# Performance work log

Measured on AMD Instinct MI355X. Metric: run time of the kernel, lower is better.

## Reference

```python
import jax, jax.numpy as jnp
import numpy as np

N_NODES = 100000


def gcn_layer(x, W, b, src, dst, n):
    # add self loops
    loop = jnp.arange(n, dtype=src.dtype)
    s = jnp.concatenate([src, loop])
    d = jnp.concatenate([dst, loop])
    # degree computed over row (source) of edge_index with self loops,
    # matching PyG degree(row, size[0])
    deg = jax.ops.segment_sum(jnp.ones_like(s, dtype=x.dtype), s, num_segments=n)
    dinv = jax.lax.rsqrt(deg)  # self loops guarantee deg >= 1
    h = x @ W + b  # [n, out]
    norm = dinv[s] * dinv[d]  # [E+n]
    msg = norm[:, None] * h[s]  # gather from source nodes
    return jax.ops.segment_sum(msg, d, num_segments=n)  # scatter-add to targets


def setup_inputs() -> dict:
    key = jax.random.key(0)
    k1, k2, k3, k4 = jax.random.split(key, 4)
    nfeat, nhid, nclass = 512, 16, 40
    E = 3200000
    x = jax.random.normal(k1, (N_NODES, nfeat), dtype=jnp.float32)
    edge_index = jax.random.randint(k2, (2, E), 0, N_NODES, dtype=jnp.int64)
    W1 = jax.random.normal(k3, (nfeat, nhid), dtype=jnp.float32) * (1.0 / np.sqrt(nfeat))
    b1 = jnp.zeros((nhid,), dtype=jnp.float32)
    W2 = jax.random.normal(k4, (nhid, nclass), dtype=jnp.float32) * (1.0 / np.sqrt(nhid))
    b2 = jnp.zeros((nclass,), dtype=jnp.float32)
    return {"x": x, "edge_index": edge_index, "W1": W1, "b1": b1, "W2": W2, "b2": b2}


def reference(x, edge_index, W1, b1, W2, b2):
    n = x.shape[0]
    src, dst = edge_index[0], edge_index[1]
    h = gcn_layer(x, W1, b1, src, dst, n)
    h = jax.nn.relu(h)
    # dropout: eval mode (identity), matching F.dropout(training=False)
    h = gcn_layer(h, W2, b2, src, dst, n)
    return jax.nn.log_softmax(h, axis=1)
```

## Files before the change

kernel.cpp:

```cpp
#include <hip/hip_runtime.h>
#include <hip/hip_bf16.h>

#define BSH 9
#define BSZ 512
#define CAP 17408
#define CHK 4096

typedef __attribute__((ext_vector_type(8))) short bf16x8;
typedef __attribute__((ext_vector_type(4))) float f32x4;

__device__ __forceinline__ unsigned short f2bf(float f) {
    unsigned u = __float_as_uint(f);
    u += 0x7fffu + ((u >> 16) & 1u);
    return (unsigned short)(u >> 16);
}
__device__ __forceinline__ float b2f(unsigned short v) {
    return __uint_as_float((unsigned)v << 16);
}

__global__ void init_k(int* __restrict__ curD, int* __restrict__ curS, int nbk) {
    int i = threadIdx.x;
    if (i < nbk) { curD[i] = i * CAP; curS[i] = i * CAP; }
}


#define GROWS 64
#define GKC 256
#define GSTR 264

__global__ __launch_bounds__(256) void fused_gs_k(
    const float* __restrict__ X, const float* __restrict__ W, const float* __restrict__ B,
    float* __restrict__ H, int n, int nGm,
    const int* __restrict__ src, const int* __restrict__ dst, int E,
    int* __restrict__ curD, int* __restrict__ curS,
    unsigned int* __restrict__ pairs, unsigned short* __restrict__ sbuf, int nbk) {
    __shared__ char smem[GROWS * GSTR * 2];
    int t = threadIdx.x;

    if ((int)blockIdx.x < nGm) {
        unsigned short* xt = (unsigned short*)smem;
        int lane = t & 63, wave = t >> 6;
        int rowBase = blockIdx.x * GROWS;
        int bn = lane & 15;

        {
            int kt0 = t >> 4, kg0 = (t >> 2) & 3, bn0 = (t & 3) * 4;
            unsigned short frag[4][8];
#pragma unroll
            for (int j = 0; j < 8; ++j) {
                float4 w = *(const float4*)&W[(size_t)(kt0 * 32 + kg0 * 8 + j) * 16 + bn0];
                frag[0][j] = f2bf(w.x); frag[1][j] = f2bf(w.y);
                frag[2][j] = f2bf(w.z); frag[3][j] = f2bf(w.w);
            }
#pragma unroll
            for (int b = 0; b < 4; ++b)
                *(uint4*)&xt[((kt0 * 4 + kg0) * 16 + bn0 + b) * 8] = *(const uint4*)frag[b];
        }
        __syncthreads();
        bf16x8 bw[16];
#pragma unroll
        for (int kt = 0; kt < 16; ++kt)
            bw[kt] = *(const bf16x8*)&xt[(kt * 64 + lane) * 8];
        float bias = B[bn];
        __syncthreads();

        f32x4 acc = {0.f, 0.f, 0.f, 0.f};
        int srow = t >> 4, skq = t & 15;

        for (int ch = 0; ch < 2; ++ch) {
#pragma unroll
            for (int p = 0; p < 4; ++p) {
                int r = p * 16 + srow;
                int gr = rowBase + r;
                const float* xr = &X[(size_t)(gr < n ? gr : n - 1) * 512 + ch * GKC + skq * 4];
#pragma unroll
                for (int q = 0; q < 4; ++q) {
                    float4 v = *(const float4*)&xr[q * 64];
                    ushort4 u;
                    u.x = f2bf(v.x); u.y = f2bf(v.y); u.z = f2bf(v.z); u.w = f2bf(v.w);
                    *(ushort4*)&xt[r * GSTR + skq * 4 + q * 64] = u;
                }
            }
            __syncthreads();

            int rb = (wave * 16 + bn) * GSTR + (lane >> 4) * 8;
#pragma unroll
            for (int kt = 0; kt < 8; ++kt) {
                bf16x8 af = *(const bf16x8*)&xt[rb + kt * 32];
                acc = __builtin_amdgcn_mfma_f32_16x16x32_bf16(af, bw[ch * 8 + kt], acc, 0, 0, 0);
            }
            __syncthreads();
        }

        int r0 = rowBase + wave * 16 + (lane >> 4) * 4;
#pragma unroll
        for (int i = 0; i < 4; ++i) {
            int row = r0 + i;
            if (row < n) H[(size_t)row * 16 + bn] = acc[i] + bias;
        }
    } else {
        unsigned int*   stageD = (unsigned int*)smem;
        unsigned short* stageS = (unsigned short*)(smem + 16384);
        int* cntD  = (int*)(smem + 24576);
        int* cntS  = (int*)(smem + 25600);
        int* rsvD  = (int*)(smem + 26624);
        int* rsvS  = (int*)(smem + 27648);
        int* scanD = (int*)(smem + 28672);
        int* scanS = (int*)(smem + 29696);
        int* ps    = (int*)(smem + 30720);

        int bb = blockIdx.x - nGm;
        int lo = bb * CHK, hi = min(E, lo + CHK);
        bool full = (hi - lo) == CHK;

        cntD[t] = 0; cntS[t] = 0;
        __syncthreads();

        int sv[16], dv[16];
        if (full) {
#pragma unroll
            for (int j = 0; j < 16; j++) {
                int i = lo + t + j * 256;
                sv[j] = src[i]; dv[j] = dst[i];
            }
#pragma unroll
            for (int j = 0; j < 16; j++) {
                atomicAdd(&cntD[dv[j] >> BSH], 1);
                atomicAdd(&cntS[sv[j] >> BSH], 1);
            }
        } else {
            for (int i = lo + t; i < hi; i += 256) {
                atomicAdd(&cntD[dst[i] >> BSH], 1);
                atomicAdd(&cntS[src[i] >> BSH], 1);
            }
        }
        __syncthreads();
        int vD = cntD[t];
        ps[t] = vD; __syncthreads();
        for (int o = 1; o < 256; o <<= 1) {
            int u = (t >= o) ? ps[t - o] : 0; __syncthreads();
            ps[t] += u; __syncthreads();
        }
        scanD[t] = ps[t] - vD;
        if (t < nbk && vD) rsvD[t] = atomicAdd(&curD[t], vD);
        __syncthreads();
        int vS = cntS[t];
        ps[t] = vS; __syncthreads();
        for (int o = 1; o < 256; o <<= 1) {
            int u = (t >= o) ? ps[t - o] : 0; __syncthreads();
            ps[t] += u; __syncthreads();
        }
        scanS[t] = ps[t] - vS;
        if (t < nbk && vS) rsvS[t] = atomicAdd(&curS[t], vS);
        cntD[t] = 0; cntS[t] = 0;
        __syncthreads();
        if (full) {
#pragma unroll
            for (int j = 0; j < 16; j++) {
                int s = sv[j], d = dv[j];
                int bd = d >> BSH;
                int pd = scanD[bd] + atomicAdd(&cntD[bd], 1);
                stageD[pd] = ((unsigned int)s << BSH) | (unsigned int)(d & (BSZ - 1));
                int bs = s >> BSH;
                int pp = scanS[bs] + atomicAdd(&cntS[bs], 1);
                stageS[pp] = (unsigned short)(s & (BSZ - 1));
            }
        } else {
            for (int i = lo + t; i < hi; i += 256) {
                int s = src[i], d = dst[i];
                int bd = d >> BSH;
                int pd = scanD[bd] + atomicAdd(&cntD[bd], 1);
                stageD[pd] = ((unsigned int)s << BSH) | (unsigned int)(d & (BSZ - 1));
                int bs = s >> BSH;
                int pp = scanS[bs] + atomicAdd(&cntS[bs], 1);
                stageS[pp] = (unsigned short)(s & (BSZ - 1));
            }
        }
        __syncthreads();
        int wave = t >> 6, lane = t & 63;
        for (int b = wave; b < nbk; b += 4) {
            int st = scanD[b], len = cntD[b], g = rsvD[b];
            for (int j = lane; j < len; j += 64) pairs[g + j] = stageD[st + j];
        }
        for (int b = wave; b < nbk; b += 4) {
            int st = scanS[b], len = cntS[b], g = rsvS[b];
            for (int j = lane; j < len; j += 64) sbuf[g + j] = stageS[st + j];
        }
    }
}


__global__ __launch_bounds__(256) void dinvScale_k(const unsigned short* __restrict__ sbuf,
                                                   const int* __restrict__ curS,
                                                   const float* __restrict__ h1,
                                                   float* __restrict__ dinv,
                                                   unsigned short* __restrict__ hw1, int n) {
    __shared__ int cnt[BSZ];
    __shared__ float dl[BSZ];
    int b = blockIdx.x, t = threadIdx.x;
    cnt[t] = 0; cnt[t + 256] = 0;
    __syncthreads();
    int lo = b * CAP, hi = curS[b];
    for (int i = lo + t; i < hi; i += 256) atomicAdd(&cnt[sbuf[i]], 1);
    __syncthreads();
    int n0 = b * BSZ + t, n1 = n0 + 256;
    float d0 = rsqrtf((float)(1 + cnt[t]));
    float d1 = rsqrtf((float)(1 + cnt[t + 256]));
    dl[t] = d0; dl[t + 256] = d1;
    if (n0 < n) dinv[n0] = d0;
    if (n1 < n) dinv[n1] = d1;
    __syncthreads();
    int rows = min(BSZ, n - b * BSZ);
    int lim4 = rows * 4;
    size_t base = (size_t)b * BSZ * 16;
#pragma unroll
    for (int j = 0; j < 8; j++) {
        int i4 = j * 256 + t;
        if (i4 < lim4) {
            float4 v = *(const float4*)&h1[base + (size_t)i4 * 4];
            float d = dl[i4 >> 2];
            ushort4 u;
            u.x = f2bf(v.x * d); u.y = f2bf(v.y * d);
            u.z = f2bf(v.z * d); u.w = f2bf(v.w * d);
            *(ushort4*)&hw1[base + (size_t)i4 * 4] = u;
        }
    }
}


#define FPS 65536.f
#define FPI (1.f / 65536.f)

template <int LAYER>
__global__ __launch_bounds__(1024) void aggB_k(
    const unsigned int* __restrict__ pairs, const int* __restrict__ curD,
    const unsigned short* __restrict__ HW, const float* __restrict__ dinv,
    float* __restrict__ rowsum, const float* __restrict__ W2,
    const float* __restrict__ B2, unsigned short* __restrict__ outA,
    float* __restrict__ outF, int n, int nc) {
    __shared__ int iacc[BSZ * 16];
    __shared__ unsigned int rsl[BSZ];
    int b = blockIdx.x, t = threadIdx.x;
    for (int i = t; i < BSZ * 16; i += 1024) iacc[i] = 0;
    if (LAYER == 1 && t < BSZ) rsl[t] = 0u;
    __syncthreads();

    int lo = b * CAP, hi = curD[b];
    int q = t & 3;
    int i = lo + (t >> 2);
    for (; i + 768 < hi; i += 1024) {
        unsigned int p0 = pairs[i], p1 = pairs[i + 256];
        unsigned int p2 = pairs[i + 512], p3 = pairs[i + 768];
        int s0 = p0 >> BSH, l0 = p0 & (BSZ - 1);
        int s1 = p1 >> BSH, l1 = p1 & (BSZ - 1);
        int s2 = p2 >> BSH, l2 = p2 & (BSZ - 1);
        int s3 = p3 >> BSH, l3 = p3 & (BSZ - 1);
        ushort4 u0 = *(const ushort4*)&HW[(size_t)s0 * 16 + q * 4];
        ushort4 u1 = *(const ushort4*)&HW[(size_t)s1 * 16 + q * 4];
        ushort4 u2 = *(const ushort4*)&HW[(size_t)s2 * 16 + q * 4];
        ushort4 u3 = *(const ushort4*)&HW[(size_t)s3 * 16 + q * 4];
        int* a0 = &iacc[l0 * 16 + q * 4];
        atomicAdd(&a0[0], __float2int_rn(b2f(u0.x) * FPS));
        atomicAdd(&a0[1], __float2int_rn(b2f(u0.y) * FPS));
        atomicAdd(&a0[2], __float2int_rn(b2f(u0.z) * FPS));
        atomicAdd(&a0[3], __float2int_rn(b2f(u0.w) * FPS));
        int* a1 = &iacc[l1 * 16 + q * 4];
        atomicAdd(&a1[0], __float2int_rn(b2f(u1.x) * FPS));
        atomicAdd(&a1[1], __float2int_rn(b2f(u1.y) * FPS));
        atomicAdd(&a1[2], __float2int_rn(b2f(u1.z) * FPS));
        atomicAdd(&a1[3], __float2int_rn(b2f(u1.w) * FPS));
        int* a2 = &iacc[l2 * 16 + q * 4];
        atomicAdd(&a2[0], __float2int_rn(b2f(u2.x) * FPS));
        atomicAdd(&a2[1], __float2int_rn(b2f(u2.y) * FPS));
        atomicAdd(&a2[2], __float2int_rn(b2f(u2.z) * FPS));
        atomicAdd(&a2[3], __float2int_rn(b2f(u2.w) * FPS));
        int* a3 = &iacc[l3 * 16 + q * 4];
        atomicAdd(&a3[0], __float2int_rn(b2f(u3.x) * FPS));
        atomicAdd(&a3[1], __float2int_rn(b2f(u3.y) * FPS));
        atomicAdd(&a3[2], __float2int_rn(b2f(u3.z) * FPS));
        atomicAdd(&a3[3], __float2int_rn(b2f(u3.w) * FPS));
        if (LAYER == 1 && q == 0) {
            atomicAdd(&rsl[l0], (unsigned int)(dinv[s0] * FPS + 0.5f));
            atomicAdd(&rsl[l1], (unsigned int)(dinv[s1] * FPS + 0.5f));
            atomicAdd(&rsl[l2], (unsigned int)(dinv[s2] * FPS + 0.5f));
            atomicAdd(&rsl[l3], (unsigned int)(dinv[s3] * FPS + 0.5f));
        }
    }
    for (; i < hi; i += 256) {
        unsigned int p0 = pairs[i];
        int s0 = p0 >> BSH, l0 = p0 & (BSZ - 1);
        ushort4 u0 = *(const ushort4*)&HW[(size_t)s0 * 16 + q * 4];
        int* a0 = &iacc[l0 * 16 + q * 4];
        atomicAdd(&a0[0], __float2int_rn(b2f(u0.x) * FPS));
        atomicAdd(&a0[1], __float2int_rn(b2f(u0.y) * FPS));
        atomicAdd(&a0[2], __float2int_rn(b2f(u0.z) * FPS));
        atomicAdd(&a0[3], __float2int_rn(b2f(u0.w) * FPS));
        if (LAYER == 1 && q == 0) atomicAdd(&rsl[l0], (unsigned int)(dinv[s0] * FPS + 0.5f));
    }
    __syncthreads();

    if (LAYER == 1) {
        int ln = t >> 1, f0 = (t & 1) * 8;
        int node = b * BSZ + ln;
        if (node < n) {
            float dd = dinv[node];
            const ushort4* sp = (const ushort4*)&HW[(size_t)node * 16 + f0];
            ushort4 s0 = sp[0], s1 = sp[1];
            const int* ap = &iacc[ln * 16 + f0];
            ushort4 o0, o1;
            o0.x = f2bf(dd * fmaxf(dd * ((float)ap[0] * FPI + b2f(s0.x)), 0.f));
            o0.y = f2bf(dd * fmaxf(dd * ((float)ap[1] * FPI + b2f(s0.y)), 0.f));
            o0.z = f2bf(dd * fmaxf(dd * ((float)ap[2] * FPI + b2f(s0.z)), 0.f));
            o0.w = f2bf(dd * fmaxf(dd * ((float)ap[3] * FPI + b2f(s0.w)), 0.f));
            o1.x = f2bf(dd * fmaxf(dd * ((float)ap[4] * FPI + b2f(s1.x)), 0.f));
            o1.y = f2bf(dd * fmaxf(dd * ((float)ap[5] * FPI + b2f(s1.y)), 0.f));
            o1.z = f2bf(dd * fmaxf(dd * ((float)ap[6] * FPI + b2f(s1.z)), 0.f));
            o1.w = f2bf(dd * fmaxf(dd * ((float)ap[7] * FPI + b2f(s1.w)), 0.f));
            ushort4* op = (ushort4*)&outA[(size_t)node * 16 + f0];
            op[0] = o0; op[1] = o1;
            if (f0 == 0) rowsum[node] = dd * (dd + (float)rsl[ln] * FPI);
        }
    } else {
        int wave = t >> 6, lane = t & 63;
        int node0 = b * BSZ;
        int nodeEnd = min(node0 + BSZ, n);
        for (int node = node0 + wave; node < nodeEnd; node += 16) {
            int ln = node - node0;
            float dd = dinv[node];
            float f[16];
            const ushort4* sp = (const ushort4*)&HW[(size_t)node * 16];
#pragma unroll
            for (int g = 0; g < 4; g++) {
                ushort4 u = sp[g];
                f[g * 4 + 0] = dd * ((float)iacc[ln * 16 + g * 4 + 0] * FPI + b2f(u.x));
                f[g * 4 + 1] = dd * ((float)iacc[ln * 16 + g * 4 + 1] * FPI + b2f(u.y));
                f[g * 4 + 2] = dd * ((float)iacc[ln * 16 + g * 4 + 2] * FPI + b2f(u.z));
                f[g * 4 + 3] = dd * ((float)iacc[ln * 16 + g * 4 + 3] * FPI + b2f(u.w));
            }
            float logit = -1e30f;
            if (lane < nc) {
                logit = rowsum[node] * B2[lane];
#pragma unroll
                for (int k = 0; k < 16; k++) logit = fmaf(f[k], W2[k * nc + lane], logit);
            }
            float m = logit;
#pragma unroll
            for (int off = 1; off < 64; off <<= 1) m = fmaxf(m, __shfl_xor(m, off, 64));
            float e = (lane < nc) ? __expf(logit - m) : 0.f;
            float s = e;
#pragma unroll
            for (int off = 1; off < 64; off <<= 1) s += __shfl_xor(s, off, 64);
            if (lane < nc) outF[(size_t)node * nc + lane] = logit - m - __logf(s);
        }
    }
}


extern "C" void kernel_launch(void* const* d_in, const int* in_sizes, int n_in,
                              void* d_out, int out_size, void* d_ws, size_t ws_size,
                              hipStream_t stream) {
    const float* X  = (const float*)d_in[0];
    const int*   EI = (const int*)d_in[1];
    const float* W1 = (const float*)d_in[2];
    const float* B1 = (const float*)d_in[3];
    const float* W2 = (const float*)d_in[4];
    const float* B2 = (const float*)d_in[5];
    float* out = (float*)d_out;

    int NH = in_sizes[3];
    int NC = in_sizes[5];
    int NF = in_sizes[2] / NH;
    int n  = in_sizes[0] / NF;
    int E  = in_sizes[1] / 2;
    const int* src = EI;
    const int* dst = EI + E;
    int nbk = (n + BSZ - 1) >> BSH;

    char* ws = (char*)d_ws;
    size_t o = 0;
    auto alloc = [&](size_t bytes) { size_t r = o; o = (o + bytes + 255) & ~(size_t)255; return r; };
    size_t o_dinv   = alloc((size_t)n * 4);
    size_t o_rsum   = alloc((size_t)n * 4);
    size_t o_curD   = alloc(1024);
    size_t o_curS   = alloc(1024);
    size_t o_pairs  = alloc((size_t)nbk * CAP * 4);
    size_t o_sbuf   = alloc((size_t)nbk * CAP * 2);
    size_t o_h1     = alloc((size_t)n * 16 * 4);
    size_t o_hw1    = alloc((size_t)n * 16 * 2);
    size_t o_a1w    = alloc((size_t)n * 16 * 2);

    float* dinv  = (float*)(ws + o_dinv);
    float* rsum  = (float*)(ws + o_rsum);
    int* curD    = (int*)(ws + o_curD);
    int* curS    = (int*)(ws + o_curS);
    unsigned int* pairs   = (unsigned int*)(ws + o_pairs);
    unsigned short* sbuf  = (unsigned short*)(ws + o_sbuf);
    float* h1    = (float*)(ws + o_h1);
    unsigned short* hw1 = (unsigned short*)(ws + o_hw1);
    unsigned short* a1w = (unsigned short*)(ws + o_a1w);

    init_k<<<1, 256, 0, stream>>>(curD, curS, nbk);

    int NBLK = (E + CHK - 1) / CHK;
    int nGm = (n + GROWS - 1) / GROWS;
    fused_gs_k<<<nGm + NBLK, 256, 0, stream>>>(X, W1, B1, h1, n, nGm,
                                               src, dst, E, curD, curS,
                                               pairs, sbuf, nbk);
    dinvScale_k<<<nbk, 256, 0, stream>>>(sbuf, curS, h1, dinv, hw1, n);

    aggB_k<1><<<nbk, 1024, 0, stream>>>(pairs, curD, hw1, dinv, rsum,
                                        nullptr, nullptr, a1w, nullptr, n, NC);
    aggB_k<2><<<nbk, 1024, 0, stream>>>(pairs, curD, a1w, dinv, rsum,
                                        W2, B2, nullptr, out, n, NC);
}
```

Before: 197.9 us.

## Split fused GEMM/scatter kernel and use shuffle-based block scan

```diff
diff --git a/kernel.cpp b/kernel.cpp
--- a/kernel.cpp
+++ b/kernel.cpp
@@ -23,169 +23,177 @@
     if (i < nbk) { curD[i] = i * CAP; curS[i] = i * CAP; }
 }
 
+__device__ __forceinline__ int blockExclScan(int v, int t, int* wsum) {
+    int lane = t & 63, wv = t >> 6;
+    int x = v;
+#pragma unroll
+    for (int off = 1; off < 64; off <<= 1) {
+        int y = __shfl_up(x, off, 64);
+        if (lane >= off) x += y;
+    }
+    if (lane == 63) wsum[wv] = x;
+    __syncthreads();
+    int prefix = 0;
+#pragma unroll
+    for (int w = 0; w < 4; ++w) prefix += (w < wv) ? wsum[w] : 0;
+    return x + prefix - v;
+}
+
+
+__global__ __launch_bounds__(256) void scatter_k(
+    const int* __restrict__ src, const int* __restrict__ dst, int E,
+    int* __restrict__ curD, int* __restrict__ curS,
+    unsigned int* __restrict__ pairs, unsigned short* __restrict__ sbuf, int nbk) {
+    __shared__ char smem[32512];
+    unsigned int*   stageD = (unsigned int*)smem;
+    unsigned short* stageS = (unsigned short*)(smem + 16384);
+    int* cntD  = (int*)(smem + 24576);
+    int* cntS  = (int*)(smem + 25600);
+    int* rsvD  = (int*)(smem + 26624);
+    int* rsvS  = (int*)(smem + 27648);
+    int* scanD = (int*)(smem + 28672);
+    int* scanS = (int*)(smem + 29696);
+    int* wsum  = (int*)(smem + 30720);
+    int t = threadIdx.x;
+
+    int lo = blockIdx.x * CHK, hi = min(E, lo + CHK);
+    bool full = (hi - lo) == CHK;
+
+    cntD[t] = 0; cntS[t] = 0;
+    __syncthreads();
+
+    int sv[16], dv[16];
+    if (full) {
+#pragma unroll
+        for (int j = 0; j < 16; j++) {
+            int i = lo + t + j * 256;
+            sv[j] = src[i]; dv[j] = dst[i];
+        }
+#pragma unroll
+        for (int j = 0; j < 16; j++) {
+            atomicAdd(&cntD[dv[j] >> BSH], 1);
+            atomicAdd(&cntS[sv[j] >> BSH], 1);
+        }
+    } else {
+        for (int i = lo + t; i < hi; i += 256) {
+            atomicAdd(&cntD[dst[i] >> BSH], 1);
+            atomicAdd(&cntS[src[i] >> BSH], 1);
+        }
+    }
+    __syncthreads();
+    int vD = cntD[t];
+    int vS = cntS[t];
+    int eD = blockExclScan(vD, t, wsum);
+    __syncthreads();
+    int eS = blockExclScan(vS, t, wsum);
+    scanD[t] = eD;
+    scanS[t] = eS;
+    if (t < nbk && vD) rsvD[t] = atomicAdd(&curD[t], vD);
+    if (t < nbk && vS) rsvS[t] = atomicAdd(&curS[t], vS);
+    cntD[t] = 0; cntS[t] = 0;
+    __syncthreads();
+    if (full) {
+#pragma unroll
+        for (int j = 0; j < 16; j++) {
+            int s = sv[j], d = dv[j];
+            int bd = d >> BSH;
+            int pd = scanD[bd] + atomicAdd(&cntD[bd], 1);
+            stageD[pd] = ((unsigned int)s << BSH) | (unsigned int)(d & (BSZ - 1));
+            int bs = s >> BSH;
+            int pp = scanS[bs] + atomicAdd(&cntS[bs], 1);
+            stageS[pp] = (unsigned short)(s & (BSZ - 1));
+        }
+    } else {
+        for (int i = lo + t; i < hi; i += 256) {
+            int s = src[i], d = dst[i];
+            int bd = d >> BSH;
+            int pd = scanD[bd] + atomicAdd(&cntD[bd], 1);
+            stageD[pd] = ((unsigned int)s << BSH) | (unsigned int)(d & (BSZ - 1));
+            int bs = s >> BSH;
+            int pp = scanS[bs] + atomicAdd(&cntS[bs], 1);
+            stageS[pp] = (unsigned short)(s & (BSZ - 1));
+        }
+    }
+    __syncthreads();
+    int wave = t >> 6, lane = t & 63;
+    for (int b = wave; b < nbk; b += 4) {
+        int st = scanD[b], len = cntD[b], g = rsvD[b];
+        for (int j = lane; j < len; j += 64) pairs[g + j] = stageD[st + j];
+    }
+    for (int b = wave; b < nbk; b += 4) {
+        int st = scanS[b], len = cntS[b], g = rsvS[b];
+        for (int j = lane; j < len; j += 64) sbuf[g + j] = stageS[st + j];
+    }
+}
+
 
 #define GROWS 64
 #define GKC 256
 #define GSTR 264
 
-__global__ __launch_bounds__(256) void fused_gs_k(
+__global__ __launch_bounds__(256) void gemm_k(
     const float* __restrict__ X, const float* __restrict__ W, const float* __restrict__ B,
-    float* __restrict__ H, int n, int nGm,
-    const int* __restrict__ src, const int* __restrict__ dst, int E,
-    int* __restrict__ curD, int* __restrict__ curS,
-    unsigned int* __restrict__ pairs, unsigned short* __restrict__ sbuf, int nbk) {
-    __shared__ char smem[GROWS * GSTR * 2];
+    float* __restrict__ H, int n) {
+    __shared__ unsigned short xt[GROWS * GSTR];
     int t = threadIdx.x;
-
-    if ((int)blockIdx.x < nGm) {
-        unsigned short* xt = (unsigned short*)smem;
-        int lane = t & 63, wave = t >> 6;
-        int rowBase = blockIdx.x * GROWS;
-        int bn = lane & 15;
-
-        {
-            int kt0 = t >> 4, kg0 = (t >> 2) & 3, bn0 = (t & 3) * 4;
-            unsigned short frag[4][8];
-#pragma unroll
-            for (int j = 0; j < 8; ++j) {
-                float4 w = *(const float4*)&W[(size_t)(kt0 * 32 + kg0 * 8 + j) * 16 + bn0];
-                frag[0][j] = f2bf(w.x); frag[1][j] = f2bf(w.y);
-                frag[2][j] = f2bf(w.z); frag[3][j] = f2bf(w.w);
+    int lane = t & 63, wave = t >> 6;
+    int rowBase = blockIdx.x * GROWS;
+    int bn = lane & 15;
+
+    {
+        int kt0 = t >> 4, kg0 = (t >> 2) & 3, bn0 = (t & 3) * 4;
+        unsigned short frag[4][8];
+#pragma unroll
+        for (int j = 0; j < 8; ++j) {
+            float4 w = *(const float4*)&W[(size_t)(kt0 * 32 + kg0 * 8 + j) * 16 + bn0];
+            frag[0][j] = f2bf(w.x); frag[1][j] = f2bf(w.y);
+            frag[2][j] = f2bf(w.z); frag[3][j] = f2bf(w.w);
+        }
+#pragma unroll
+        for (int b = 0; b < 4; ++b)
+            *(uint4*)&xt[((kt0 * 4 + kg0) * 16 + bn0 + b) * 8] = *(const uint4*)frag[b];
+    }
+    __syncthreads();
+    bf16x8 bw[16];
+#pragma unroll
+    for (int kt = 0; kt < 16; ++kt)
+        bw[kt] = *(const bf16x8*)&xt[(kt * 64 + lane) * 8];
+    float bias = B[bn];
+    __syncthreads();
+
+    f32x4 acc = {0.f, 0.f, 0.f, 0.f};
+    int srow = t >> 4, skq = t & 15;
+
+    for (int ch = 0; ch < 2; ++ch) {
+#pragma unroll
+        for (int p = 0; p < 4; ++p) {
+            int r = p * 16 + srow;
+            int gr = rowBase + r;
+            const float* xr = &X[(size_t)(gr < n ? gr : n - 1) * 512 + ch * GKC + skq * 4];
+#pragma unroll
+            for (int q = 0; q < 4; ++q) {
+                float4 v = *(const float4*)&xr[q * 64];
+                ushort4 u;
+                u.x = f2bf(v.x); u.y = f2bf(v.y); u.z = f2bf(v.z); u.w = f2bf(v.w);
+                *(ushort4*)&xt[r * GSTR + skq * 4 + q * 64] = u;
             }
-#pragma unroll
-            for (int b = 0; b < 4; ++b)
-                *(uint4*)&xt[((kt0 * 4 + kg0) * 16 + bn0 + b) * 8] = *(const uint4*)frag[b];
         }
         __syncthreads();
-        bf16x8 bw[16];
-#pragma unroll
-        for (int kt = 0; kt < 16; ++kt)
-            bw[kt] = *(const bf16x8*)&xt[(kt * 64 + lane) * 8];
-        float bias = B[bn];
+
+        int rb = (wave * 16 + bn) * GSTR + (lane >> 4) * 8;
+#pragma unroll
+        for (int kt = 0; kt < 8; ++kt) {
+            bf16x8 af = *(const bf16x8*)&xt[rb + kt * 32];
+            acc = __builtin_amdgcn_mfma_f32_16x16x32_bf16(af, bw[ch * 8 + kt], acc, 0, 0, 0);
+        }
         __syncthreads();
-
-        f32x4 acc = {0.f, 0.f, 0.f, 0.f};
-        int srow = t >> 4, skq = t & 15;
-
-        for (int ch = 0; ch < 2; ++ch) {
-#pragma unroll
-            for (int p = 0; p < 4; ++p) {
-                int r = p * 16 + srow;
-                int gr = rowBase + r;
-                const float* xr = &X[(size_t)(gr < n ? gr : n - 1) * 512 + ch * GKC + skq * 4];
-#pragma unroll
-                for (int q = 0; q < 4; ++q) {
-                    float4 v = *(const float4*)&xr[q * 64];
-                    ushort4 u;
-                    u.x = f2bf(v.x); u.y = f2bf(v.y); u.z = f2bf(v.z); u.w = f2bf(v.w);
-                    *(ushort4*)&xt[r * GSTR + skq * 4 + q * 64] = u;
-                }
-            }
-            __syncthreads();
-
-            int rb = (wave * 16 + bn) * GSTR + (lane >> 4) * 8;
-#pragma unroll
-            for (int kt = 0; kt < 8; ++kt) {
-                bf16x8 af = *(const bf16x8*)&xt[rb + kt * 32];
-                acc = __builtin_amdgcn_mfma_f32_16x16x32_bf16(af, bw[ch * 8 + kt], acc, 0, 0, 0);
-            }
-            __syncthreads();
-        }
-
-        int r0 = rowBase + wave * 16 + (lane >> 4) * 4;
-#pragma unroll
-        for (int i = 0; i < 4; ++i) {
-            int row = r0 + i;
-            if (row < n) H[(size_t)row * 16 + bn] = acc[i] + bias;
-        }
-    } else {
-        unsigned int*   stageD = (unsigned int*)smem;
-        unsigned short* stageS = (unsigned short*)(smem + 16384);
-        int* cntD  = (int*)(smem + 24576);
-        int* cntS  = (int*)(smem + 25600);
-        int* rsvD  = (int*)(smem + 26624);
-        int* rsvS  = (int*)(smem + 27648);
-        int* scanD = (int*)(smem + 28672);
-        int* scanS = (int*)(smem + 29696);
-        int* ps    = (int*)(smem + 30720);
-
-        int bb = blockIdx.x - nGm;
-        int lo = bb * CHK, hi = min(E, lo + CHK);
-        bool full = (hi - lo) == CHK;
-
-        cntD[t] = 0; cntS[t] = 0;
-        __syncthreads();
-
-        int sv[16], dv[16];
-        if (full) {
-#pragma unroll
-            for (int j = 0; j < 16; j++) {
-                int i = lo + t + j * 256;
-                sv[j] = src[i]; dv[j] = dst[i];
-            }
-#pragma unroll
-            for (int j = 0; j < 16; j++) {
-                atomicAdd(&cntD[dv[j] >> BSH], 1);
-                atomicAdd(&cntS[sv[j] >> BSH], 1);
-            }
-        } else {
-            for (int i = lo + t; i < hi; i += 256) {
-                atomicAdd(&cntD[dst[i] >> BSH], 1);
-                atomicAdd(&cntS[src[i] >> BSH], 1);
-            }
-        }
-        __syncthreads();
-        int vD = cntD[t];
-        ps[t] = vD; __syncthreads();
-        for (int o = 1; o < 256; o <<= 1) {
-            int u = (t >= o) ? ps[t - o] : 0; __syncthreads();
-            ps[t] += u; __syncthreads();
-        }
-        scanD[t] = ps[t] - vD;
-        if (t < nbk && vD) rsvD[t] = atomicAdd(&curD[t], vD);
-        __syncthreads();
-        int vS = cntS[t];
-        ps[t] = vS; __syncthreads();
-        for (int o = 1; o < 256; o <<= 1) {
-            int u = (t >= o) ? ps[t - o] : 0; __syncthreads();
-            ps[t] += u; __syncthreads();
-        }
-        scanS[t] = ps[t] - vS;
-        if (t < nbk && vS) rsvS[t] = atomicAdd(&curS[t], vS);
-        cntD[t] = 0; cntS[t] = 0;
-        __syncthreads();
-        if (full) {
-#pragma unroll
-            for (int j = 0; j < 16; j++) {
-                int s = sv[j], d = dv[j];
-                int bd = d >> BSH;
-                int pd = scanD[bd] + atomicAdd(&cntD[bd], 1);
-                stageD[pd] = ((unsigned int)s << BSH) | (unsigned int)(d & (BSZ - 1));
-                int bs = s >> BSH;
-                int pp = scanS[bs] + atomicAdd(&cntS[bs], 1);
-                stageS[pp] = (unsigned short)(s & (BSZ - 1));
-            }
-        } else {
-            for (int i = lo + t; i < hi; i += 256) {
-                int s = src[i], d = dst[i];
-                int bd = d >> BSH;
-                int pd = scanD[bd] + atomicAdd(&cntD[bd], 1);
-                stageD[pd] = ((unsigned int)s << BSH) | (unsigned int)(d & (BSZ - 1));
-                int bs = s >> BSH;
-                int pp = scanS[bs] + atomicAdd(&cntS[bs], 1);
-                stageS[pp] = (unsigned short)(s & (BSZ - 1));
-            }
-        }
-        __syncthreads();
-        int wave = t >> 6, lane = t & 63;
-        for (int b = wave; b < nbk; b += 4) {
-            int st = scanD[b], len = cntD[b], g = rsvD[b];
-            for (int j = lane; j < len; j += 64) pairs[g + j] = stageD[st + j];
-        }
-        for (int b = wave; b < nbk; b += 4) {
-            int st = scanS[b], len = cntS[b], g = rsvS[b];
-            for (int j = lane; j < len; j += 64) sbuf[g + j] = stageS[st + j];
-        }
+    }
+
+    int r0 = rowBase + wave * 16 + (lane >> 4) * 4;
+#pragma unroll
+    for (int i = 0; i < 4; ++i) {
+        int row = r0 + i;
+        if (row < n) H[(size_t)row * 16 + bn] = acc[i] + bias;
     }
 }
 
@@ -403,9 +411,8 @@
 
     int NBLK = (E + CHK - 1) / CHK;
     int nGm = (n + GROWS - 1) / GROWS;
-    fused_gs_k<<<nGm + NBLK, 256, 0, stream>>>(X, W1, B1, h1, n, nGm,
-                                               src, dst, E, curD, curS,
-                                               pairs, sbuf, nbk);
+    scatter_k<<<NBLK, 256, 0, stream>>>(src, dst, E, curD, curS, pairs, sbuf, nbk);
+    gemm_k<<<nGm, 256, 0, stream>>>(X, W1, B1, h1, n);
     dinvScale_k<<<nbk, 256, 0, stream>>>(sbuf, curS, h1, dinv, hw1, n);
 
     aggB_k<1><<<nbk, 1024, 0, stream>>>(pairs, curD, hw1, dinv, rsum,
```

After: 211.7 us. +7.0%, slower.
